# Optimization experiments

Measured on AMD Instinct MI355X. Metric: run time of the kernel, lower is better.

Reference implementation:

```python
import jax, jax.numpy as jnp
import numpy as np
from jax import lax

N_FREQ = 25
T = 524289
T_MAX = 10.0


def setup_inputs() -> dict:
    key = jax.random.key(0)
    k1, k2 = jax.random.split(key, 2)
    t = jnp.arange(T, dtype=jnp.float32) * np.float32(T_MAX / T)
    x0 = jax.random.normal(k1, (2,), dtype=jnp.float32)
    freqs = jnp.arange(1, N_FREQ + 1, dtype=jnp.float32)
    # xavier_normal with gain=0.3: std = 0.3*sqrt(2/(fan_in+fan_out)) = 0.3*sqrt(2/54)
    std = np.float32(0.3 * np.sqrt(2.0 / (2 * N_FREQ + 4)))
    W = jax.random.normal(k2, (4, 2 * N_FREQ), dtype=jnp.float32) * std
    b = jnp.zeros((4,), dtype=jnp.float32)
    return {"t": t, "x0": x0, "freqs": freqs, "W": W, "b": b}


def _expm2x2(M):
    """Closed-form matrix exponential of a batch of 2x2 matrices M (..., 2, 2).
    exp(M) = e^mu (cosh(s) I + sinhc(s) N), N = M - mu*I, s^2 = mu^2 - det(M).
    Handles s^2 < 0 (rotation) via cos/sinc, and s^2 ~ 0 via Taylor series."""
    a = M[..., 0, 0]
    b = M[..., 0, 1]
    c = M[..., 1, 0]
    d = M[..., 1, 1]
    mu = 0.5 * (a + d)
    p = 0.5 * (a - d)          # traceless part diagonal
    s2 = p * p + b * c          # s^2 (can be negative)
    abs_s2 = jnp.abs(s2)
    tiny = jnp.float32(1e-24)
    small = abs_s2 < jnp.float32(1e-12)
    sq = jnp.sqrt(jnp.where(small, tiny, abs_s2))
    pos = s2 >= 0
    cosh_ = jnp.where(small, 1.0 + 0.5 * s2,
                      jnp.where(pos, jnp.cosh(sq), jnp.cos(sq)))
    sinhc = jnp.where(small, 1.0 + s2 / 6.0,
                      jnp.where(pos, jnp.sinh(sq) / sq, jnp.sin(sq) / sq))
    em = jnp.exp(mu)
    e00 = em * (cosh_ + sinhc * p)
    e01 = em * (sinhc * b)
    e10 = em * (sinhc * c)
    e11 = em * (cosh_ - sinhc * p)
    return jnp.stack([jnp.stack([e00, e01], -1), jnp.stack([e10, e11], -1)], -2)


def _forward(t, x0, freqs, W, b):
    def A_of(ts):  # ts: (N,) -> (N, 2, 2)
        ph = ts[:, None] * freqs[None, :]              # (N, F)
        feat = jnp.concatenate([jnp.cos(ph), jnp.sin(ph)], axis=-1)  # (N, 2F)
        return (feat @ W.T + b).reshape(-1, 2, 2)

    t0 = t[:-1]
    t1 = t[1:]
    dt = (t1 - t0)[:, None, None]                       # (T-1, 1, 1)
    A0 = A_of(t0)
    A1 = A_of(t1)
    Am = A_of(0.5 * (t0 + t1))
    comm = A0 @ A1 - A1 @ A0                            # commutator [A0, A1]
    Omega = Am * dt + (dt * dt / 12.0) * comm           # Magnus 2nd order
    E = _expm2x2(Omega)                                 # (T-1, 2, 2)
    # cumulative left-product P_i = E_i @ ... @ E_1 via parallel scan
    P = lax.associative_scan(lambda x, y: jnp.matmul(y, x), E)
    xs = jnp.einsum('tij,j->ti', P, x0)                 # (T-1, 2)
    return jnp.concatenate([x0[None, :], xs], axis=0)   # (T, 2)


def reference(t, x0, freqs, W, b):
    return _forward(t, x0, freqs, W, b)
```

## Files before the change

### kernel.cpp

```cpp
#include <hip/hip_runtime.h>


#define NFREQ   25
#define NI      524288
#define THREADS 1024
#define BLOCKS  256
#define CPT     2
#define NTH     (THREADS * BLOCKS)
#define NWAVES  (THREADS / 64)
#define TSTEP   ((float)(10.0 / 524289.0))

struct M22 { float a, b, c, d; };

__device__ __forceinline__ M22 mmul(const M22 X, const M22 Y) {
    M22 r;
    r.a = fmaf(X.a, Y.a, X.b * Y.c);
    r.b = fmaf(X.a, Y.b, X.b * Y.d);
    r.c = fmaf(X.c, Y.a, X.d * Y.c);
    r.d = fmaf(X.c, Y.b, X.d * Y.d);
    return r;
}

__device__ __forceinline__ M22 shfl_up_m(const M22 m, int off) {
    M22 r;
    r.a = __shfl_up(m.a, off);
    r.b = __shfl_up(m.b, off);
    r.c = __shfl_up(m.c, off);
    r.d = __shfl_up(m.d, off);
    return r;
}

__device__ __forceinline__ M22 make_E(float A0, float A1, float A2, float A3,
                                      float dtv) {
    float oa = A0 * dtv, ob = A1 * dtv, oc = A2 * dtv, od = A3 * dtv;
    float mu = 0.5f * (oa + od);
    float p  = 0.5f * (oa - od);
    float s2 = fmaf(p, p, ob * oc);
    float ch  = fmaf(0.5f, s2, 1.0f);
    float shc = fmaf(0.16666667f, s2, 1.0f);
    float em = __expf(mu);
    M22 E;
    E.a = em * fmaf(shc,  p, ch);
    E.b = em * (shc * ob);
    E.c = em * (shc * oc);
    E.d = em * fmaf(shc, -p, ch);
    return E;
}

__global__ __launch_bounds__(THREADS) void k_agg(
        const float* __restrict__ W, const float* __restrict__ b,
        M22* __restrict__ blockTot, float4* __restrict__ Lout) {
    __shared__ __align__(16) float Wl[NFREQ * 8];
    __shared__ float bl[4];
    __shared__ M22 waveTot[NWAVES];
    __shared__ M22 wavePre[NWAVES];

    const int tid  = threadIdx.x;
    const int bid  = blockIdx.x;
    const int lane = tid & 63;
    const int wid  = tid >> 6;

    if (tid < NFREQ * 8) {
        int j = tid >> 3, m = tid & 7, r = m & 3, part = m >> 2;
        Wl[tid] = W[r * 50 + part * 25 + j];
    }
    if (tid < 4) bl[tid] = b[tid];
    __syncthreads();

    const int gtid = bid * THREADS + tid;
    const int i0   = gtid * CPT;
    const float t0 = (float)(i0)     * TSTEP;
    const float t1 = (float)(i0 + 1) * TSTEP;
    const float t2 = (float)(i0 + 2) * TSTEP;

    const float tmA = 0.5f * (t0 + t1);
    const float tmB = 0.5f * (t1 + t2);
    const float c1A = __cosf(tmA), s1A = __sinf(tmA);
    const float c1B = __cosf(tmB), s1B = __sinf(tmB);
    const float tcA = c1A + c1A, tcB = c1B + c1B;

    float cjA = c1A, cmA = 1.0f, sjA = s1A, smA = 0.0f;
    float cjB = c1B, cmB = 1.0f, sjB = s1B, smB = 0.0f;
    const float b0 = bl[0], b1 = bl[1], b2 = bl[2], b3 = bl[3];
    float aA0 = b0, aA1 = b1, aA2 = b2, aA3 = b3;
    float aB0 = b0, aB1 = b1, aB2 = b2, aB3 = b3;

#pragma unroll
    for (int j = 0; j < NFREQ; j++) {
        const float4 wc = *reinterpret_cast<const float4*>(&Wl[j * 8]);
        const float4 ws = *reinterpret_cast<const float4*>(&Wl[j * 8 + 4]);
        aA0 = fmaf(cjA, wc.x, aA0);  aA1 = fmaf(cjA, wc.y, aA1);
        aA2 = fmaf(cjA, wc.z, aA2);  aA3 = fmaf(cjA, wc.w, aA3);
        aA0 = fmaf(sjA, ws.x, aA0);  aA1 = fmaf(sjA, ws.y, aA1);
        aA2 = fmaf(sjA, ws.z, aA2);  aA3 = fmaf(sjA, ws.w, aA3);
        aB0 = fmaf(cjB, wc.x, aB0);  aB1 = fmaf(cjB, wc.y, aB1);
        aB2 = fmaf(cjB, wc.z, aB2);  aB3 = fmaf(cjB, wc.w, aB3);
        aB0 = fmaf(sjB, ws.x, aB0);  aB1 = fmaf(sjB, ws.y, aB1);
        aB2 = fmaf(sjB, ws.z, aB2);  aB3 = fmaf(sjB, ws.w, aB3);
        float cnA = fmaf(tcA, cjA, -cmA), snA = fmaf(tcA, sjA, -smA);
        float cnB = fmaf(tcB, cjB, -cmB), snB = fmaf(tcB, sjB, -smB);
        cmA = cjA; cjA = cnA;  smA = sjA; sjA = snA;
        cmB = cjB; cjB = cnB;  smB = sjB; sjB = snB;
    }

    const M22 E0 = make_E(aA0, aA1, aA2, aA3, t1 - t0);
    const M22 E1 = make_E(aB0, aB1, aB2, aB3, t2 - t1);
    M22 Mth = mmul(E1, E0);

    M22 inc = Mth;
#pragma unroll
    for (int off = 1; off < 64; off <<= 1) {
        M22 u = shfl_up_m(inc, off);
        if (lane >= off) inc = mmul(inc, u);
    }
    if (lane == 63) waveTot[wid] = inc;
    __syncthreads();

    if (wid == 0 && lane < NWAVES) {
        M22 m = waveTot[lane];
#pragma unroll
        for (int off = 1; off < NWAVES; off <<= 1) {
            M22 u = shfl_up_m(m, off);
            if (lane >= off) m = mmul(m, u);
        }
        if (lane == 0) wavePre[0] = M22{1.f, 0.f, 0.f, 1.f};
        if (lane < NWAVES - 1) wavePre[lane + 1] = m;
        if (lane == NWAVES - 1) blockTot[bid] = m;
    }
    __syncthreads();

    M22 Wex = wavePre[wid];
    M22 Texw = shfl_up_m(inc, 1);
    if (lane == 0) Texw = M22{1.f, 0.f, 0.f, 1.f};
    M22 L = mmul(Texw, Wex);

    M22 L0 = mmul(E0, L);
    Lout[0 * NTH + gtid] = make_float4(L0.a, L0.b, L0.c, L0.d);
    M22 L1 = mmul(E1, L0);
    Lout[1 * NTH + gtid] = make_float4(L1.a, L1.b, L1.c, L1.d);
}

__global__ __launch_bounds__(THREADS) void k_apply(
        const float* __restrict__ x0,
        const M22* __restrict__ blockTot,
        const float4* __restrict__ Lin,
        float* __restrict__ out) {
    __shared__ M22 sInc[BLOCKS];
    __shared__ M22 segTot[4];
    __shared__ float wvec[2];

    const int tid  = threadIdx.x;
    const int bid  = blockIdx.x;
    const int lane = tid & 63;
    const int wid  = tid >> 6;

    if (tid < BLOCKS) {
        M22 binc = blockTot[tid];
#pragma unroll
        for (int off = 1; off < 64; off <<= 1) {
            M22 u = shfl_up_m(binc, off);
            if (lane >= off) binc = mmul(binc, u);
        }
        sInc[tid] = binc;
        if (lane == 63) segTot[wid] = binc;
    }
    __syncthreads();
    if (tid == 0) {
        const int q = bid >> 6, r = bid & 63;
        M22 P = {1.f, 0.f, 0.f, 1.f};
        for (int s = 0; s < q; s++) P = mmul(segTot[s], P);
        if (r > 0) P = mmul(sInc[bid - 1], P);
        const float x00 = x0[0], x01 = x0[1];
        wvec[0] = fmaf(P.a, x00, P.b * x01);
        wvec[1] = fmaf(P.c, x00, P.d * x01);
    }
    __syncthreads();

    const float w0 = wvec[0], w1 = wvec[1];
    const int gtid = bid * THREADS + tid;
    const int i0   = gtid * CPT;
    float2* out2 = reinterpret_cast<float2*>(out);
#pragma unroll
    for (int k = 0; k < CPT; k++) {
        float4 Lv = Lin[k * NTH + gtid];
        float v0 = fmaf(Lv.x, w0, Lv.y * w1);
        float v1 = fmaf(Lv.z, w0, Lv.w * w1);
        out2[i0 + k + 1] = make_float2(v0, v1);
    }
    if (bid == 0 && tid == 0) out2[0] = make_float2(x0[0], x0[1]);
}

extern "C" void kernel_launch(void* const* d_in, const int* in_sizes, int n_in,
                              void* d_out, int out_size, void* d_ws, size_t ws_size,
                              hipStream_t stream) {
    const float* x0 = (const float*)d_in[1];
    const float* W  = (const float*)d_in[3];
    const float* b  = (const float*)d_in[4];
    float* out      = (float*)d_out;

    char* ws = (char*)d_ws;
    M22*    blockTot = (M22*)ws;
    float4* Lbuf     = (float4*)(ws + 4096);

    k_agg<<<BLOCKS, THREADS, 0, stream>>>(W, b, blockTot, Lbuf);
    k_apply<<<BLOCKS, THREADS, 0, stream>>>(x0, blockTot, Lbuf, out);
}
```

Baseline: 16.82 us.

## Recompute per-thread scan in apply kernel instead of storing L matrices

Instead of writing per-element prefix matrices (two float4 per thread, about 8 MB) to workspace and reading them back in the second kernel, the apply kernel recomputes the Fourier features, the exponentials and the intra-block scan, then applies the block prefix vector directly. The first kernel now only emits block totals. W is read from global memory directly instead of staged in LDS. This trades an extra round of ALU and scan work for removing a large HBM write and read.

```diff
diff --git a/kernel.cpp b/kernel.cpp
--- a/kernel.cpp
+++ b/kernel.cpp
@@ -6,7 +6,6 @@
 #define THREADS 1024
 #define BLOCKS  256
 #define CPT     2
-#define NTH     (THREADS * BLOCKS)
 #define NWAVES  (THREADS / 64)
 #define TSTEP   ((float)(10.0 / 524289.0))
 
@@ -47,26 +46,14 @@
     return E;
 }
 
-__global__ __launch_bounds__(THREADS) void k_agg(
+struct Phase1 {
+    M22 E0, E1, inc;
+};
+
+__device__ __forceinline__ Phase1 phase1_body(
         const float* __restrict__ W, const float* __restrict__ b,
-        M22* __restrict__ blockTot, float4* __restrict__ Lout) {
-    __shared__ __align__(16) float Wl[NFREQ * 8];
-    __shared__ float bl[4];
-    __shared__ M22 waveTot[NWAVES];
-    __shared__ M22 wavePre[NWAVES];
-
-    const int tid  = threadIdx.x;
-    const int bid  = blockIdx.x;
-    const int lane = tid & 63;
-    const int wid  = tid >> 6;
-
-    if (tid < NFREQ * 8) {
-        int j = tid >> 3, m = tid & 7, r = m & 3, part = m >> 2;
-        Wl[tid] = W[r * 50 + part * 25 + j];
-    }
-    if (tid < 4) bl[tid] = b[tid];
-    __syncthreads();
-
+        int bid, int tid, int lane, int wid,
+        M22* waveTot, M22* wavePre, M22* blockTotOut ) {
     const int gtid = bid * THREADS + tid;
     const int i0   = gtid * CPT;
     const float t0 = (float)(i0)     * TSTEP;
@@ -81,38 +68,40 @@
 
     float cjA = c1A, cmA = 1.0f, sjA = s1A, smA = 0.0f;
     float cjB = c1B, cmB = 1.0f, sjB = s1B, smB = 0.0f;
-    const float b0 = bl[0], b1 = bl[1], b2 = bl[2], b3 = bl[3];
-    float aA0 = b0, aA1 = b1, aA2 = b2, aA3 = b3;
-    float aB0 = b0, aB1 = b1, aB2 = b2, aB3 = b3;
+    float aA0 = b[0], aA1 = b[1], aA2 = b[2], aA3 = b[3];
+    float aB0 = aA0, aB1 = aA1, aB2 = aA2, aB3 = aA3;
 
 #pragma unroll
     for (int j = 0; j < NFREQ; j++) {
-        const float4 wc = *reinterpret_cast<const float4*>(&Wl[j * 8]);
-        const float4 ws = *reinterpret_cast<const float4*>(&Wl[j * 8 + 4]);
-        aA0 = fmaf(cjA, wc.x, aA0);  aA1 = fmaf(cjA, wc.y, aA1);
-        aA2 = fmaf(cjA, wc.z, aA2);  aA3 = fmaf(cjA, wc.w, aA3);
-        aA0 = fmaf(sjA, ws.x, aA0);  aA1 = fmaf(sjA, ws.y, aA1);
-        aA2 = fmaf(sjA, ws.z, aA2);  aA3 = fmaf(sjA, ws.w, aA3);
-        aB0 = fmaf(cjB, wc.x, aB0);  aB1 = fmaf(cjB, wc.y, aB1);
-        aB2 = fmaf(cjB, wc.z, aB2);  aB3 = fmaf(cjB, wc.w, aB3);
-        aB0 = fmaf(sjB, ws.x, aB0);  aB1 = fmaf(sjB, ws.y, aB1);
-        aB2 = fmaf(sjB, ws.z, aB2);  aB3 = fmaf(sjB, ws.w, aB3);
+        const float wc0 = W[j],       wc1 = W[ 50 + j];
+        const float wc2 = W[100 + j], wc3 = W[150 + j];
+        const float ws0 = W[ 25 + j], ws1 = W[ 75 + j];
+        const float ws2 = W[125 + j], ws3 = W[175 + j];
+        aA0 = fmaf(cjA, wc0, aA0);  aA1 = fmaf(cjA, wc1, aA1);
+        aA2 = fmaf(cjA, wc2, aA2);  aA3 = fmaf(cjA, wc3, aA3);
+        aA0 = fmaf(sjA, ws0, aA0);  aA1 = fmaf(sjA, ws1, aA1);
+        aA2 = fmaf(sjA, ws2, aA2);  aA3 = fmaf(sjA, ws3, aA3);
+        aB0 = fmaf(cjB, wc0, aB0);  aB1 = fmaf(cjB, wc1, aB1);
+        aB2 = fmaf(cjB, wc2, aB2);  aB3 = fmaf(cjB, wc3, aB3);
+        aB0 = fmaf(sjB, ws0, aB0);  aB1 = fmaf(sjB, ws1, aB1);
+        aB2 = fmaf(sjB, ws2, aB2);  aB3 = fmaf(sjB, ws3, aB3);
         float cnA = fmaf(tcA, cjA, -cmA), snA = fmaf(tcA, sjA, -smA);
         float cnB = fmaf(tcB, cjB, -cmB), snB = fmaf(tcB, sjB, -smB);
         cmA = cjA; cjA = cnA;  smA = sjA; sjA = snA;
         cmB = cjB; cjB = cnB;  smB = sjB; sjB = snB;
     }
 
-    const M22 E0 = make_E(aA0, aA1, aA2, aA3, t1 - t0);
-    const M22 E1 = make_E(aB0, aB1, aB2, aB3, t2 - t1);
-    M22 Mth = mmul(E1, E0);
-
-    M22 inc = Mth;
+    Phase1 r;
+    r.E0 = make_E(aA0, aA1, aA2, aA3, t1 - t0);
+    r.E1 = make_E(aB0, aB1, aB2, aB3, t2 - t1);
+
+    M22 inc = mmul(r.E1, r.E0);
 #pragma unroll
     for (int off = 1; off < 64; off <<= 1) {
         M22 u = shfl_up_m(inc, off);
         if (lane >= off) inc = mmul(inc, u);
     }
+    r.inc = inc;
     if (lane == 63) waveTot[wid] = inc;
     __syncthreads();
 
@@ -125,26 +114,31 @@
         }
         if (lane == 0) wavePre[0] = M22{1.f, 0.f, 0.f, 1.f};
         if (lane < NWAVES - 1) wavePre[lane + 1] = m;
-        if (lane == NWAVES - 1) blockTot[bid] = m;
+        if (blockTotOut && lane == NWAVES - 1) *blockTotOut = m;
     }
     __syncthreads();
-
-    M22 Wex = wavePre[wid];
-    M22 Texw = shfl_up_m(inc, 1);
-    if (lane == 0) Texw = M22{1.f, 0.f, 0.f, 1.f};
-    M22 L = mmul(Texw, Wex);
-
-    M22 L0 = mmul(E0, L);
-    Lout[0 * NTH + gtid] = make_float4(L0.a, L0.b, L0.c, L0.d);
-    M22 L1 = mmul(E1, L0);
-    Lout[1 * NTH + gtid] = make_float4(L1.a, L1.b, L1.c, L1.d);
+    return r;
+}
+
+__global__ __launch_bounds__(THREADS) void k_agg(
+        const float* __restrict__ W, const float* __restrict__ b,
+        M22* __restrict__ blockTot) {
+    __shared__ M22 waveTot[NWAVES];
+    __shared__ M22 wavePre[NWAVES];
+    const int tid  = threadIdx.x;
+    const int bid  = blockIdx.x;
+    const int lane = tid & 63;
+    const int wid  = tid >> 6;
+    (void)phase1_body(W, b, bid, tid, lane, wid, waveTot, wavePre, &blockTot[bid]);
 }
 
 __global__ __launch_bounds__(THREADS) void k_apply(
+        const float* __restrict__ W, const float* __restrict__ b,
         const float* __restrict__ x0,
         const M22* __restrict__ blockTot,
-        const float4* __restrict__ Lin,
         float* __restrict__ out) {
+    __shared__ M22 waveTot[NWAVES];
+    __shared__ M22 wavePre[NWAVES];
     __shared__ M22 sInc[BLOCKS];
     __shared__ M22 segTot[4];
     __shared__ float wvec[2];
@@ -174,18 +168,29 @@
         wvec[0] = fmaf(P.a, x00, P.b * x01);
         wvec[1] = fmaf(P.c, x00, P.d * x01);
     }
-    __syncthreads();
-
-    const float w0 = wvec[0], w1 = wvec[1];
-    const int gtid = bid * THREADS + tid;
-    const int i0   = gtid * CPT;
+
+    Phase1 ph = phase1_body(W, b, bid, tid, lane, wid, waveTot, wavePre, nullptr);
+
+    M22 Wex  = wavePre[wid];
+    M22 Texw = shfl_up_m(ph.inc, 1);
+    if (lane == 0) Texw = M22{1.f, 0.f, 0.f, 1.f};
+
+    float v0 = wvec[0], v1 = wvec[1];
+    { float u0 = fmaf(Wex.a,  v0, Wex.b  * v1), u1 = fmaf(Wex.c,  v0, Wex.d  * v1); v0 = u0; v1 = u1; }
+    { float u0 = fmaf(Texw.a, v0, Texw.b * v1), u1 = fmaf(Texw.c, v0, Texw.d * v1); v0 = u0; v1 = u1; }
+
+    const int i0 = (bid * THREADS + tid) * CPT;
     float2* out2 = reinterpret_cast<float2*>(out);
-#pragma unroll
-    for (int k = 0; k < CPT; k++) {
-        float4 Lv = Lin[k * NTH + gtid];
-        float v0 = fmaf(Lv.x, w0, Lv.y * w1);
-        float v1 = fmaf(Lv.z, w0, Lv.w * w1);
-        out2[i0 + k + 1] = make_float2(v0, v1);
+    {
+        float u0 = fmaf(ph.E0.a, v0, ph.E0.b * v1);
+        float u1 = fmaf(ph.E0.c, v0, ph.E0.d * v1);
+        v0 = u0; v1 = u1;
+        out2[i0 + 1] = make_float2(v0, v1);
+    }
+    {
+        float u0 = fmaf(ph.E1.a, v0, ph.E1.b * v1);
+        float u1 = fmaf(ph.E1.c, v0, ph.E1.d * v1);
+        out2[i0 + 2] = make_float2(u0, u1);
     }
     if (bid == 0 && tid == 0) out2[0] = make_float2(x0[0], x0[1]);
 }
@@ -198,10 +203,8 @@
     const float* b  = (const float*)d_in[4];
     float* out      = (float*)d_out;
 
-    char* ws = (char*)d_ws;
-    M22*    blockTot = (M22*)ws;
-    float4* Lbuf     = (float4*)(ws + 4096);
-
-    k_agg<<<BLOCKS, THREADS, 0, stream>>>(W, b, blockTot, Lbuf);
-    k_apply<<<BLOCKS, THREADS, 0, stream>>>(x0, blockTot, Lbuf, out);
-}
+    M22* blockTot = (M22*)d_ws;
+
+    k_agg<<<BLOCKS, THREADS, 0, stream>>>(W, b, blockTot);
+    k_apply<<<BLOCKS, THREADS, 0, stream>>>(W, b, x0, blockTot, out);
+}
```

Result: slower. 22.37 us (+33.0%).
